# Optimization experiments

Measured on AMD Instinct MI355X. Metric: run time of the kernel, lower is better.

## Reference

```python
import jax, jax.numpy as jnp
import numpy as np

N_QUBITS = 20
N_TERMS = 4
BATCH = 16
DIM = 2 ** N_QUBITS


def _apply_two_qubit_gate(state, U, q0, q1):
    """Apply batched 4x4 unitary U (B,4,4) to qubit axes (q0,q1) of state (2,)*n+(B,)."""
    s = jnp.moveaxis(state, (q0, q1), (0, 1))
    rest = s.shape[2:-1]
    B = s.shape[-1]
    s = s.reshape(4, -1, B)  # (4, rest, B)
    out = jnp.einsum('bij,jrb->irb', U, s)
    out = out.reshape((2, 2) + rest + (B,))
    return jnp.moveaxis(out, (0, 1), (q0, q1))


def setup_inputs() -> dict:
    key = jax.random.key(0)
    k1, k2, k3, k4, k5 = jax.random.split(key, 5)
    H_real = jax.random.normal(k1, (N_TERMS, 4, 4), jnp.float32)
    H_imag = jax.random.normal(k2, (N_TERMS, 4, 4), jnp.float32)
    tevo = jax.random.uniform(k3, (N_TERMS, BATCH), jnp.float32)
    state_real = jax.random.normal(k4, (DIM, BATCH), jnp.float32)
    state_imag = jax.random.normal(k5, (DIM, BATCH), jnp.float32)
    nrm = jnp.sqrt(jnp.sum(state_real ** 2 + state_imag ** 2, axis=0, keepdims=True))
    return {'H_real': H_real, 'H_imag': H_imag, 'tevo': tevo,
            'state_real': state_real / nrm, 'state_imag': state_imag / nrm}


def reference(H_real, H_imag, tevo, state_real, state_imag):
    # Hermitian generators per term: H_k = (A + A^H)/2, A = H_real + i*H_imag  -> (K,4,4)
    A = H_real + 1j * H_imag
    H = 0.5 * (A + jnp.conj(jnp.swapaxes(A, -1, -2)))
    # Hamiltonian evolution U_k(t) = exp(-i H_k t) via eigendecomposition (HEvoPyQOperation)
    w, V = jnp.linalg.eigh(H)                       # w: (K,4) real, V: (K,4,4)
    phases = jnp.exp(-1j * w[:, None, :] * tevo[:, :, None])  # (K,B,4)
    U = jnp.einsum('kij,kbj,klj->kbil', V, phases, jnp.conj(V))  # (K,B,4,4)
    # statevector (2,)*n + (B,)
    state = (state_real + 1j * state_imag).reshape((2,) * N_QUBITS + (BATCH,))
    # AddPyQOperation: reduce(add, (op(state, values) for op in operations))
    out = jnp.zeros_like(state)
    for k in range(N_TERMS):
        out = out + _apply_two_qubit_gate(state, U[k], k, k + 1)
    out = out.reshape(DIM, BATCH)
    return jnp.stack([jnp.real(out), jnp.imag(out)])  # (2, DIM, B) real view of complex output
```

## Files before the change

kernel.cpp:

```cpp
#include <hip/hip_runtime.h>

#define NQ 20
#define DIMQ (1 << NQ)
#define NB 16
#define NT 4
#define RBITS 15
#define NCOL (1 << (RBITS + 4))

#define USTRIDE 36
#define UTOT (64 * USTRIDE)

__device__ __forceinline__ void cfma(float2& o, const float2 u, const float2 s) {
  asm("v_pk_fma_f32 %0, %1, %2, %0 op_sel_hi:[0,1,1]\n\t"
      "v_pk_fma_f32 %0, %1, %2, %0 op_sel:[1,1,0] op_sel_hi:[1,0,1] neg_lo:[1,0,0]"
      : "+v"(o) : "v"(u), "v"(s));
}
__device__ __forceinline__ float2 cmul(const float2 u, const float2 s) {
  float2 o;
  asm("v_pk_mul_f32 %0, %1, %2 op_sel_hi:[0,1]\n\t"
      "v_pk_fma_f32 %0, %1, %2, %0 op_sel:[1,1,0] op_sel_hi:[1,0,1] neg_lo:[1,0,0]"
      : "=&v"(o) : "v"(u), "v"(s));
  return o;
}

__global__ __launch_bounds__(256) void compute_u_kernel(
    const float* __restrict__ Hre, const float* __restrict__ Him,
    const float* __restrict__ tevo, float* __restrict__ uout) {
  __shared__ float er_s[64][4][4];
  __shared__ float ei_s[64][4][4];

  const int tid  = threadIdx.x;
  const int task = tid >> 2;
  const int row  = tid & 3;
  const int k    = task >> 4;
  const int b    = task & 15;

  float Ar[4][4], Ai[4][4];
#pragma unroll
  for (int i = 0; i < 4; i++) {
#pragma unroll
    for (int j = 0; j < 4; j++) {
      Ar[i][j] = Hre[k * 16 + i * 4 + j];
      Ai[i][j] = Him[k * 16 + i * 4 + j];
    }
  }
  const float t = tevo[k * NB + b];
  const float ts = t * (1.0f / 16.0f);

  float Gr[4][4], Gi[4][4];
#pragma unroll
  for (int i = 0; i < 4; i++) {
#pragma unroll
    for (int j = 0; j < 4; j++) {
      const float hr = 0.5f * (Ar[i][j] + Ar[j][i]);
      const float hi = 0.5f * (Ai[i][j] - Ai[j][i]);
      Gr[i][j] = ts * hi;
      Gi[i][j] = -ts * hr;
    }
  }

  float Er[4], Ei[4], Tr[4], Ti[4];
#pragma unroll
  for (int j = 0; j < 4; j++) {
    Er[j] = (j == row) ? 1.0f : 0.0f;
    Ei[j] = 0.0f;
    Tr[j] = Er[j];
    Ti[j] = 0.0f;
  }
#pragma unroll
  for (int m = 1; m <= 8; m++) {
    const float inv = 1.0f / (float)m;
    float nr[4], ni[4];
#pragma unroll
    for (int j = 0; j < 4; j++) {
      float ar = 0.0f, ai = 0.0f;
#pragma unroll
      for (int p = 0; p < 4; p++) {
        ar += Tr[p] * Gr[p][j] - Ti[p] * Gi[p][j];
        ai += Tr[p] * Gi[p][j] + Ti[p] * Gr[p][j];
      }
      nr[j] = ar * inv;
      ni[j] = ai * inv;
    }
#pragma unroll
    for (int j = 0; j < 4; j++) {
      Tr[j] = nr[j]; Ti[j] = ni[j];
      Er[j] += nr[j]; Ei[j] += ni[j];
    }
  }

  for (int q = 0; q < 4; q++) {
    __syncthreads();
#pragma unroll
    for (int j = 0; j < 4; j++) {
      er_s[task][row][j] = Er[j];
      ei_s[task][row][j] = Ei[j];
    }
    __syncthreads();
    float nr[4], ni[4];
#pragma unroll
    for (int j = 0; j < 4; j++) {
      float ar = 0.0f, ai = 0.0f;
#pragma unroll
      for (int p = 0; p < 4; p++) {
        ar += Er[p] * er_s[task][p][j] - Ei[p] * ei_s[task][p][j];
        ai += Er[p] * ei_s[task][p][j] + Ei[p] * er_s[task][p][j];
      }
      nr[j] = ar; ni[j] = ai;
    }
#pragma unroll
    for (int j = 0; j < 4; j++) { Er[j] = nr[j]; Ei[j] = ni[j]; }
  }

  const int ubase = (k * 16 + b) * USTRIDE;
#pragma unroll
  for (int j = 0; j < 4; j++) {
    uout[ubase + (row * 4 + j) * 2]     = Er[j];
    uout[ubase + (row * 4 + j) * 2 + 1] = Ei[j];
  }
}

__global__ __launch_bounds__(256, 4) void apply_gates_kernel(
    const float* __restrict__ sre, const float* __restrict__ sim,
    const float* __restrict__ u, float* __restrict__ out) {
  __shared__ __align__(16) float ul[UTOT];
  __shared__ __align__(16) float st[64 * 64];
  const int tid = threadIdx.x;
  const int w   = tid >> 6;
  const int l   = tid & 63;
  const int c0  = blockIdx.x * 64;
  const int b   = l & 15;
  const int q0  = w & 1;

#pragma unroll
  for (int t = 0; t < 4; t++) {
    const int p  = w * 4 + t;
    const int pl = p * 4 + (l >> 4);
    const int g  = pl & 31;
    const float* src = (pl < 32 ? sre : sim) + (g << 19) + c0 + (l & 15) * 4;
    float* dst = st + p * 256;
    __builtin_amdgcn_global_load_lds(
        (const __attribute__((address_space(1))) float*)(const void*)src,
        (__attribute__((address_space(3))) float*)(void*)dst, 16, 0, 0);
  }

#pragma unroll
  for (int q = 0; q < 9; q++) ul[tid + q * 256] = u[tid + q * 256];

  __syncthreads();

  float2 s[8];
#pragma unroll
  for (int m = 0; m < 8; m++) {
    s[m].x = st[(w * 8 + m) * 64 + l];
    s[m].y = st[(32 + w * 8 + m) * 64 + l];
  }

  float2 o[8];

  {
    const float* ub = &ul[(3 * 16 + b) * USTRIDE];
#pragma unroll
    for (int i = 0; i < 4; i++) {
      const float4 v0 = *(const float4*)(ub + i * 8);
      const float4 v1 = *(const float4*)(ub + i * 8 + 4);
      const float2 u0 = make_float2(v0.x, v0.y), u1 = make_float2(v0.z, v0.w);
      const float2 u2 = make_float2(v1.x, v1.y), u3 = make_float2(v1.z, v1.w);
#pragma unroll
      for (int h = 0; h < 2; h++) {
        const int om = h * 4 + i;
        o[om] = cmul(u0, s[h * 4 + 0]);
        cfma(o[om], u1, s[h * 4 + 1]);
        cfma(o[om], u2, s[h * 4 + 2]);
        cfma(o[om], u3, s[h * 4 + 3]);
      }
    }
  }

  {
    const float* ub = &ul[(2 * 16 + b) * USTRIDE];
#pragma unroll
    for (int i = 0; i < 4; i++) {
      const float4 v0 = *(const float4*)(ub + i * 8);
      const float4 v1 = *(const float4*)(ub + i * 8 + 4);
      const float2 u0 = make_float2(v0.x, v0.y), u1 = make_float2(v0.z, v0.w);
      const float2 u2 = make_float2(v1.x, v1.y), u3 = make_float2(v1.z, v1.w);
#pragma unroll
      for (int l0 = 0; l0 < 2; l0++) {
        const int om = i * 2 + l0;
        cfma(o[om], u0, s[l0]);
        cfma(o[om], u1, s[2 + l0]);
        cfma(o[om], u2, s[4 + l0]);
        cfma(o[om], u3, s[6 + l0]);
      }
    }
  }

  {
    float2 p[8];
    const int pq = w ^ 1;
#pragma unroll
    for (int m = 0; m < 8; m++) {
      p[m].x = st[(pq * 8 + m) * 64 + l];
      p[m].y = st[(32 + pq * 8 + m) * 64 + l];
    }
    const float* ub1 = &ul[(1 * 16 + b) * USTRIDE];
#pragma unroll
    for (int mh = 0; mh < 2; mh++) {
      const int i = q0 * 2 + mh;
      const float* row = ub1 + i * 8;
#pragma unroll
      for (int j2 = 0; j2 < 2; j2++) {
        const float2 uo = *(const float2*)(row + (q0 * 2 + j2) * 2);
        const float2 up = *(const float2*)(row + ((q0 ^ 1) * 2 + j2) * 2);
#pragma unroll
        for (int ml = 0; ml < 4; ml++) {
          const int om = mh * 4 + ml;
          cfma(o[om], uo, s[j2 * 4 + ml]);
          cfma(o[om], up, p[j2 * 4 + ml]);
        }
      }
    }
    const float* ub0 = &ul[b * USTRIDE];
    const float2 u01 = *(const float2*)(ub0 + (w * 4 + (w ^ 1)) * 2);
#pragma unroll
    for (int m = 0; m < 8; m++) cfma(o[m], u01, p[m]);
  }

  {
    const float* ub0 = &ul[b * USTRIDE];
    const float2 u00 = *(const float2*)(ub0 + (w * 4 + w) * 2);
#pragma unroll
    for (int m = 0; m < 8; m++) cfma(o[m], u00, s[m]);
#pragma unroll
    for (int d = 2; d < 4; d++) {
      const int jq = w ^ d;
      const float2 uj = *(const float2*)(ub0 + (w * 4 + jq) * 2);
#pragma unroll
      for (int m = 0; m < 8; m++) {
        float2 t;
        t.x = st[(jq * 8 + m) * 64 + l];
        t.y = st[(32 + jq * 8 + m) * 64 + l];
        cfma(o[m], uj, t);
      }
    }
  }

#pragma unroll
  for (int m = 0; m < 8; m++) {
    const int off = c0 + l + ((w * 8 + m) << 19);
    __builtin_nontemporal_store(o[m].x, out + off);
    __builtin_nontemporal_store(o[m].y, out + off + (1 << 24));
  }
}

extern "C" void kernel_launch(void* const* d_in, const int* in_sizes, int n_in,
                              void* d_out, int out_size, void* d_ws, size_t ws_size,
                              hipStream_t stream) {
  const float* Hre  = (const float*)d_in[0];
  const float* Him  = (const float*)d_in[1];
  const float* tevo = (const float*)d_in[2];
  const float* sre  = (const float*)d_in[3];
  const float* sim  = (const float*)d_in[4];
  float* out = (float*)d_out;
  float* uws = (float*)d_ws;

  compute_u_kernel<<<1, 256, 0, stream>>>(Hre, Him, tevo, uws);
  apply_gates_kernel<<<NCOL / 64, 256, 0, stream>>>(sre, sim, uws, out);
}
```

Baseline: 51.14 us.

## Process two 64-column chunks per block to amortize unitary loads

Each block now handles 128 columns instead of 64, holding two independent state tiles (A and B) per thread and reusing each loaded unitary coefficient across both. The shared staging buffer doubles to 32KB, the async global-to-LDS load is restructured so each wave loads 8 rows of 512 bytes, and the grid is halved. This amortizes the per-block U table copy and LDS coefficient reads and adds instruction-level parallelism, at the cost of more registers and more LDS, which may lower occupancy under the 4-blocks-per-CU launch bound.

```diff
diff --git a/kernel.cpp b/kernel.cpp
--- a/kernel.cpp
+++ b/kernel.cpp
@@ -124,21 +124,20 @@
     const float* __restrict__ sre, const float* __restrict__ sim,
     const float* __restrict__ u, float* __restrict__ out) {
   __shared__ __align__(16) float ul[UTOT];
-  __shared__ __align__(16) float st[64 * 64];
+  __shared__ __align__(16) float st[32 * 256];
   const int tid = threadIdx.x;
   const int w   = tid >> 6;
   const int l   = tid & 63;
-  const int c0  = blockIdx.x * 64;
+  const int c0  = blockIdx.x * 128;
   const int b   = l & 15;
   const int q0  = w & 1;
 
 #pragma unroll
-  for (int t = 0; t < 4; t++) {
-    const int p  = w * 4 + t;
-    const int pl = p * 4 + (l >> 4);
-    const int g  = pl & 31;
-    const float* src = (pl < 32 ? sre : sim) + (g << 19) + c0 + (l & 15) * 4;
-    float* dst = st + p * 256;
+  for (int t = 0; t < 8; t++) {
+    const int g = w * 8 + t;
+    const float* base = (l < 32) ? sre : sim;
+    const float* src  = base + (g << 19) + c0 + (l & 31) * 4;
+    float* dst = st + g * 256;
     __builtin_amdgcn_global_load_lds(
         (const __attribute__((address_space(1))) float*)(const void*)src,
         (__attribute__((address_space(3))) float*)(void*)dst, 16, 0, 0);
@@ -149,14 +148,15 @@
 
   __syncthreads();
 
-  float2 s[8];
+  float2 sA[8], sB[8];
 #pragma unroll
   for (int m = 0; m < 8; m++) {
-    s[m].x = st[(w * 8 + m) * 64 + l];
-    s[m].y = st[(32 + w * 8 + m) * 64 + l];
-  }
-
-  float2 o[8];
+    const int a = (w * 8 + m) * 256 + l;
+    sA[m].x = st[a];       sA[m].y = st[a + 128];
+    sB[m].x = st[a + 64];  sB[m].y = st[a + 192];
+  }
+
+  float2 oA[8], oB[8];
 
   {
     const float* ub = &ul[(3 * 16 + b) * USTRIDE];
@@ -169,10 +169,14 @@
 #pragma unroll
       for (int h = 0; h < 2; h++) {
         const int om = h * 4 + i;
-        o[om] = cmul(u0, s[h * 4 + 0]);
-        cfma(o[om], u1, s[h * 4 + 1]);
-        cfma(o[om], u2, s[h * 4 + 2]);
-        cfma(o[om], u3, s[h * 4 + 3]);
+        oA[om] = cmul(u0, sA[h * 4 + 0]);
+        cfma(oA[om], u1, sA[h * 4 + 1]);
+        cfma(oA[om], u2, sA[h * 4 + 2]);
+        cfma(oA[om], u3, sA[h * 4 + 3]);
+        oB[om] = cmul(u0, sB[h * 4 + 0]);
+        cfma(oB[om], u1, sB[h * 4 + 1]);
+        cfma(oB[om], u2, sB[h * 4 + 2]);
+        cfma(oB[om], u3, sB[h * 4 + 3]);
       }
     }
   }
@@ -188,69 +192,87 @@
 #pragma unroll
       for (int l0 = 0; l0 < 2; l0++) {
         const int om = i * 2 + l0;
-        cfma(o[om], u0, s[l0]);
-        cfma(o[om], u1, s[2 + l0]);
-        cfma(o[om], u2, s[4 + l0]);
-        cfma(o[om], u3, s[6 + l0]);
-      }
-    }
-  }
-
-  {
-    float2 p[8];
-    const int pq = w ^ 1;
-#pragma unroll
-    for (int m = 0; m < 8; m++) {
-      p[m].x = st[(pq * 8 + m) * 64 + l];
-      p[m].y = st[(32 + pq * 8 + m) * 64 + l];
-    }
+        cfma(oA[om], u0, sA[l0]);
+        cfma(oA[om], u1, sA[2 + l0]);
+        cfma(oA[om], u2, sA[4 + l0]);
+        cfma(oA[om], u3, sA[6 + l0]);
+        cfma(oB[om], u0, sB[l0]);
+        cfma(oB[om], u1, sB[2 + l0]);
+        cfma(oB[om], u2, sB[4 + l0]);
+        cfma(oB[om], u3, sB[6 + l0]);
+      }
+    }
+  }
+
+  {
     const float* ub1 = &ul[(1 * 16 + b) * USTRIDE];
-#pragma unroll
-    for (int mh = 0; mh < 2; mh++) {
-      const int i = q0 * 2 + mh;
-      const float* row = ub1 + i * 8;
-#pragma unroll
-      for (int j2 = 0; j2 < 2; j2++) {
-        const float2 uo = *(const float2*)(row + (q0 * 2 + j2) * 2);
-        const float2 up = *(const float2*)(row + ((q0 ^ 1) * 2 + j2) * 2);
-#pragma unroll
-        for (int ml = 0; ml < 4; ml++) {
-          const int om = mh * 4 + ml;
-          cfma(o[om], uo, s[j2 * 4 + ml]);
-          cfma(o[om], up, p[j2 * 4 + ml]);
-        }
-      }
-    }
     const float* ub0 = &ul[b * USTRIDE];
     const float2 u01 = *(const float2*)(ub0 + (w * 4 + (w ^ 1)) * 2);
-#pragma unroll
-    for (int m = 0; m < 8; m++) cfma(o[m], u01, p[m]);
+    const int pq = w ^ 1;
+#pragma unroll
+    for (int cs = 0; cs < 2; cs++) {
+      float2* o = cs ? oB : oA;
+      float2* s = cs ? sB : sA;
+      const int co = cs * 64;
+      float2 p[8];
+#pragma unroll
+      for (int m = 0; m < 8; m++) {
+        const int a = (pq * 8 + m) * 256 + l + co;
+        p[m].x = st[a];
+        p[m].y = st[a + 128];
+      }
+#pragma unroll
+      for (int mh = 0; mh < 2; mh++) {
+        const int i = q0 * 2 + mh;
+        const float* row = ub1 + i * 8;
+#pragma unroll
+        for (int j2 = 0; j2 < 2; j2++) {
+          const float2 uo = *(const float2*)(row + (q0 * 2 + j2) * 2);
+          const float2 up = *(const float2*)(row + ((q0 ^ 1) * 2 + j2) * 2);
+#pragma unroll
+          for (int ml = 0; ml < 4; ml++) {
+            const int om = mh * 4 + ml;
+            cfma(o[om], uo, s[j2 * 4 + ml]);
+            cfma(o[om], up, p[j2 * 4 + ml]);
+          }
+        }
+      }
+#pragma unroll
+      for (int m = 0; m < 8; m++) cfma(o[m], u01, p[m]);
+    }
   }
 
   {
     const float* ub0 = &ul[b * USTRIDE];
     const float2 u00 = *(const float2*)(ub0 + (w * 4 + w) * 2);
 #pragma unroll
-    for (int m = 0; m < 8; m++) cfma(o[m], u00, s[m]);
+    for (int m = 0; m < 8; m++) {
+      cfma(oA[m], u00, sA[m]);
+      cfma(oB[m], u00, sB[m]);
+    }
 #pragma unroll
     for (int d = 2; d < 4; d++) {
       const int jq = w ^ d;
       const float2 uj = *(const float2*)(ub0 + (w * 4 + jq) * 2);
 #pragma unroll
       for (int m = 0; m < 8; m++) {
-        float2 t;
-        t.x = st[(jq * 8 + m) * 64 + l];
-        t.y = st[(32 + jq * 8 + m) * 64 + l];
-        cfma(o[m], uj, t);
+        const int a = (jq * 8 + m) * 256 + l;
+        float2 tA, tB;
+        tA.x = st[a];       tA.y = st[a + 128];
+        tB.x = st[a + 64];  tB.y = st[a + 192];
+        cfma(oA[m], uj, tA);
+        cfma(oB[m], uj, tB);
       }
     }
   }
 
 #pragma unroll
   for (int m = 0; m < 8; m++) {
-    const int off = c0 + l + ((w * 8 + m) << 19);
-    __builtin_nontemporal_store(o[m].x, out + off);
-    __builtin_nontemporal_store(o[m].y, out + off + (1 << 24));
+    const int offA = c0 + l + ((w * 8 + m) << 19);
+    __builtin_nontemporal_store(oA[m].x, out + offA);
+    __builtin_nontemporal_store(oA[m].y, out + offA + (1 << 24));
+    __builtin_nontemporal_store(oB[m].x, out + offA + 64);
+    __builtin_nontemporal_store(oB[m].y, out + offA + 64 + (1 << 24));
   }
 }
 
@@ -266,5 +288,5 @@
   float* uws = (float*)d_ws;
 
   compute_u_kernel<<<1, 256, 0, stream>>>(Hre, Him, tevo, uws);
-  apply_gates_kernel<<<NCOL / 64, 256, 0, stream>>>(sre, sim, uws, out);
-}
+  apply_gates_kernel<<<NCOL / 128, 256, 0, stream>>>(sre, sim, uws, out);
+}
```

New measurement: 52.26 us. 1.02x slower.
